# Kernel tuning notes

Hardware: AMD Instinct MI355X
Metric: run time of the kernel (lower is better)

Reference implementation:

```python
import jax, jax.numpy as jnp
import numpy as np

B, T, C, H, MAX_LEN = 16, 512, 1024, 16, 512
D = C // H  # head_dim = 64

def setup_inputs() -> dict:
    key = jax.random.key(0)
    ks = jax.random.split(key, 10)
    s = 1.0 / np.sqrt(C)
    return {
        "x": jax.random.normal(ks[0], (B, T, C), dtype=jnp.float32),
        "Wq": jax.random.normal(ks[1], (C, C), dtype=jnp.float32) * s,
        "bq": jnp.zeros((C,), dtype=jnp.float32),
        "Wk": jax.random.normal(ks[2], (C, C), dtype=jnp.float32) * s,
        "bk": jnp.zeros((C,), dtype=jnp.float32),
        "Wv": jax.random.normal(ks[3], (C, C), dtype=jnp.float32) * s,
        "bv": jnp.zeros((C,), dtype=jnp.float32),
        "Wo": jax.random.normal(ks[4], (C, C), dtype=jnp.float32) * s,
        "bo": jnp.zeros((C,), dtype=jnp.float32),
        "rel_pos_bias": jax.random.normal(ks[5], (H, MAX_LEN, MAX_LEN), dtype=jnp.float32) * 0.02,
    }

def reference(x, Wq, bq, Wk, bk, Wv, bv, Wo, bo, rel_pos_bias):
    scale = 1.0 / jnp.sqrt(jnp.float32(D))
    # projections (torch Linear: x @ W.T + b), reshape to (B,H,T,D)
    def proj(W, b):
        return (x @ W.T + b).reshape(B, T, H, D).transpose(0, 2, 1, 3)
    q, k, v = proj(Wq, bq), proj(Wk, bk), proj(Wv, bv)
    attn = jnp.einsum('bhtd,bhsd->bhts', q, k) * scale  # (B,H,T,T)
    attn = attn + rel_pos_bias[None, :, :T, :T]
    causal = jnp.triu(jnp.ones((T, T), dtype=bool), k=1)
    attn = jnp.where(causal[None, None], -jnp.inf, attn)
    attn = jax.nn.softmax(attn, axis=-1)  # dropout p=0 (eval) -> identity
    out = jnp.einsum('bhts,bhsd->bhtd', attn, v)
    out = out.transpose(0, 2, 1, 3).reshape(B, T, C)
    return out @ Wo.T + bo
```

## Files before the change

### kernel.cpp

```cpp
#include <hip/hip_runtime.h>
#include <stdint.h>
#include <math.h>

#define DEV static __device__ __forceinline__

typedef __attribute__((ext_vector_type(8))) __bf16 bf16x8;
typedef __attribute__((ext_vector_type(4))) float f32x4;
typedef unsigned short u16;

DEV u16 f2b(float f) {
  union { float f; uint32_t u; } x; x.f = f;
  uint32_t r = x.u + 0x7fffu + ((x.u >> 16) & 1u);
  return (u16)(r >> 16);
}

DEV uint32_t pk2(float a, float b) {
  return (uint32_t)f2b(a) | ((uint32_t)f2b(b) << 16);
}

DEV float b2f_lo(uint32_t u) { return __uint_as_float(u << 16); }
DEV float b2f_hi(uint32_t u) { return __uint_as_float(u & 0xffff0000u); }

DEV void glds16(const void* g, void* l) {
  __builtin_amdgcn_global_load_lds(
      (const __attribute__((address_space(1))) void*)g,
      (__attribute__((address_space(3))) void*)l, 16, 0, 0);
}

DEV f32x4 mfma16(bf16x8 a, bf16x8 b, f32x4 c) {
  return __builtin_amdgcn_mfma_f32_16x16x32_bf16(a, b, c, 0, 0, 0);
}

__global__ __launch_bounds__(256) void cvt_all(
    const float* __restrict__ x, const float* __restrict__ Wq,
    const float* __restrict__ Wk, const float* __restrict__ Wv,
    const float* __restrict__ Wo, const float* __restrict__ bias,
    u16* __restrict__ xb, u16* __restrict__ wqkv, u16* __restrict__ wo,
    u16* __restrict__ biasb) {
  size_t i = ((size_t)blockIdx.x * 256 + threadIdx.x) * 4;
  const float* s;
  u16* d;
  size_t off;
  float scale = 1.0f;
  if (i < 8388608)        { s = x;  d = xb;             off = i; }
  else if (i < 9437184)   { s = Wq; d = wqkv;           off = i - 8388608; }
  else if (i < 10485760)  { s = Wk; d = wqkv + 1048576; off = i - 9437184; }
  else if (i < 11534336)  { s = Wv; d = wqkv + 2097152; off = i - 10485760; }
  else if (i < 12582912)  { s = Wo; d = wo;             off = i - 11534336; }
  else { s = bias; d = biasb; off = i - 12582912; scale = 1.44269504f; }
  float4 v = *(const float4*)(s + off);
  ushort4 o;
  o.x = f2b(v.x * scale); o.y = f2b(v.y * scale);
  o.z = f2b(v.z * scale); o.w = f2b(v.w * scale);
  *(ushort4*)(d + off) = o;
}

__global__ __launch_bounds__(256) void gemm_qkv(
    const u16* __restrict__ A, const u16* __restrict__ Bw,
    const float* __restrict__ bq, const float* __restrict__ bk,
    const float* __restrict__ bv,
    u16* __restrict__ qo, u16* __restrict__ ko, u16* __restrict__ vto) {
  __shared__ u16 lsA[2][128 * 32];
  __shared__ u16 lsB[2][128 * 32];
  const int K = 1024;
  int tid = threadIdx.x, wave = tid >> 6, lane = tid & 63;
  int q16 = lane >> 4, c16 = lane & 15;
  int m0 = blockIdx.y * 128, n0 = blockIdx.x * 128;
  int wm = wave >> 1, wn = wave & 1;
  const bool vblk = (n0 >= 2048);
  const u16* lsR = vblk ? &lsB[0][0] : &lsA[0][0];
  const u16* lsC = vblk ? &lsA[0][0] : &lsB[0][0];
  int wr = vblk ? wn : wm;
  int wc = vblk ? wm : wn;

  f32x4 acc[4][4];
#pragma unroll
  for (int i = 0; i < 4; ++i)
#pragma unroll
    for (int j = 0; j < 4; ++j) acc[i][j] = (f32x4)0.0f;

  int srow = (lane >> 2);
  int scol = ((lane & 3) ^ ((lane >> 3) & 3)) * 8;
  int swz = (q16 ^ ((c16 >> 1) & 3)) * 8;

  for (int k0 = 0; k0 < K; k0 += 64) {
    __syncthreads();
#pragma unroll
    for (int half = 0; half < 2; ++half) {
#pragma unroll
      for (int cc = 0; cc < 2; ++cc) {
        int chunk = wave * 2 + cc;
        int r = chunk * 16 + srow;
        glds16(A + (size_t)(m0 + r) * K + k0 + half * 32 + scol,
               &lsA[half][chunk * 512]);
        glds16(Bw + (size_t)(n0 + r) * K + k0 + half * 32 + scol,
               &lsB[half][chunk * 512]);
      }
    }
    __syncthreads();
#pragma unroll
    for (int half = 0; half < 2; ++half) {
      bf16x8 rf[4], cf[4];
#pragma unroll
      for (int i = 0; i < 4; ++i)
        rf[i] = *(const bf16x8*)&lsR[half * 4096 +
                                     (wr * 64 + i * 16 + c16) * 32 + swz];
#pragma unroll
      for (int i = 0; i < 4; ++i)
        cf[i] = *(const bf16x8*)&lsC[half * 4096 +
                                     (wc * 64 + i * 16 + c16) * 32 + swz];
#pragma unroll
      for (int it = 0; it < 4; ++it)
#pragma unroll
        for (int jt = 0; jt < 4; ++jt)
          acc[it][jt] = mfma16(rf[it], cf[jt], acc[it][jt]);
    }
  }

  if (!vblk) {
#pragma unroll
    for (int mt = 0; mt < 4; ++mt) {
#pragma unroll
      for (int nt = 0; nt < 4; ++nt) {
        int n = n0 + wn * 64 + nt * 16 + c16;
        int which = n >> 10;
        int nl = n & 1023;
        int hh = nl >> 6, d = nl & 63;
        float bias = (which == 0 ? bq : bk)[nl];
        u16* dst = (which == 0 ? qo : ko);
#pragma unroll
        for (int r = 0; r < 4; ++r) {
          int m = m0 + wm * 64 + mt * 16 + q16 * 4 + r;
          int b = m >> 9, t = m & 511;
          size_t bh = (size_t)b * 16 + hh;
          dst[(bh * 512 + t) * 72 + d] = f2b(acc[mt][nt][r] + bias);
        }
      }
    }
  } else {
#pragma unroll
    for (int it = 0; it < 4; ++it) {
      int nbase = n0 + wn * 64 + it * 16 + q16 * 4;
      float4 bvv = *(const float4*)(bv + (nbase & 1023));
#pragma unroll
      for (int jt = 0; jt < 4; ++jt) {
        int m = m0 + wm * 64 + jt * 16 + c16;
        int b = m >> 9, t = m & 511;
        size_t bh4 = ((size_t)b * 16) * 4;
#pragma unroll
        for (int r = 0; r < 4; ++r) {
          int nl = (nbase + r) & 1023;
          int hh = nl >> 6, d = nl & 63;
          float bias = ((const float*)&bvv)[r];
          vto[((bh4 + (size_t)hh * 4 + (t >> 7)) * 64 + d) * 136 + (t & 127)] =
              f2b(acc[it][jt][r] + bias);
        }
      }
    }
  }
}

__global__ __launch_bounds__(256, 3) void attn_kernel(
    const u16* __restrict__ qglob, const u16* __restrict__ kglob,
    const u16* __restrict__ vtglob, const u16* __restrict__ biasb,
    u16* __restrict__ og) {
  __shared__ u16 lsK[128 * 72];
  __shared__ u16 lsV[64 * 136];
  __shared__ u16 lsP[4 * 32 * 72];

  int tid = threadIdx.x, wave = tid >> 6, lane = tid & 63;
  int q16 = lane >> 4, c16 = lane & 15;
  int bh = blockIdx.y;
  int b = bh >> 4, h = bh & 15;
  int bx = blockIdx.x;
  int q0 = bx * 128;

  const u16* qbase = qglob + (size_t)bh * (512 * 72) + (size_t)q0 * 72;
  const u16* kbase = kglob + (size_t)bh * (512 * 72);
  const u16* vbase = vtglob + (size_t)bh * 4 * (64 * 136);
  u16* lsPw = lsP + wave * (32 * 72);

  for (int i = wave; i < 18; i += 4)
    glds16(qbase + (size_t)i * 512 + lane * 8, lsK + i * 512);
  __syncthreads();
  bf16x8 qf[2][2];
#pragma unroll
  for (int nt = 0; nt < 2; ++nt)
#pragma unroll
    for (int ks = 0; ks < 2; ++ks)
      qf[nt][ks] = *(const bf16x8*)&lsK[(wave * 32 + nt * 16 + c16) * 72 +
                                        ks * 32 + q16 * 8];

  f32x4 oacc[2][4];
#pragma unroll
  for (int i = 0; i < 2; ++i)
#pragma unroll
    for (int j = 0; j < 4; ++j) oacc[i][j] = (f32x4)0.0f;
  float mold[2] = {-INFINITY, -INFINITY};
  float lsum[2] = {0.0f, 0.0f};
  const float SCL = 0.18033688f;

  for (int st = 0; st <= bx; ++st) {
    bool diag = (st == bx);
    __syncthreads();
    const u16* kt = kbase + (size_t)st * (128 * 72);
    for (int i = wave; i < 18; i += 4)
      glds16(kt + (size_t)i * 512 + lane * 8, lsK + i * 512);
    const u16* vt = vbase + (size_t)st * (64 * 136);
    for (int i = wave; i < 17; i += 4)
      glds16(vt + (size_t)i * 512 + lane * 8, lsV + i * 512);

    uint2 ub[2][8];
#pragma unroll
    for (int nt = 0; nt < 2; ++nt) {
      int qgl = q0 + wave * 32 + nt * 16 + c16;
      const u16* bp = biasb + ((size_t)h * 512 + qgl) * 512 + st * 128 + q16 * 4;
#pragma unroll
      for (int mt = 0; mt < 8; ++mt) ub[nt][mt] = *(const uint2*)(bp + mt * 16);
    }
    __syncthreads();

    f32x4 sa[8][2];
#pragma unroll
    for (int mt = 0; mt < 8; ++mt) {
      sa[mt][0] = (f32x4)0.0f;
      sa[mt][1] = (f32x4)0.0f;
    }
    int mtmax = diag ? 2 * wave + 2 : 8;
#pragma unroll
    for (int mt = 0; mt < 8; ++mt) {
      if (mt < mtmax) {
#pragma unroll
        for (int ks = 0; ks < 2; ++ks) {
          bf16x8 kf =
              *(const bf16x8*)&lsK[(mt * 16 + c16) * 72 + ks * 32 + q16 * 8];
          sa[mt][0] = mfma16(kf, qf[0][ks], sa[mt][0]);
          sa[mt][1] = mfma16(kf, qf[1][ks], sa[mt][1]);
        }
      }
    }

    float alpha[2];
#pragma unroll
    for (int nt = 0; nt < 2; ++nt) {
#pragma unroll
      for (int mt = 0; mt < 8; ++mt) {
        uint32_t lo = ub[nt][mt].x, hi = ub[nt][mt].y;
        f32x4 bv;
        bv[0] = b2f_lo(lo); bv[1] = b2f_hi(lo);
        bv[2] = b2f_lo(hi); bv[3] = b2f_hi(hi);
        sa[mt][nt] = sa[mt][nt] * SCL + bv;
      }
      if (diag) {
#pragma unroll
        for (int mt = 0; mt < 8; ++mt) {
          int d0 = mt * 16 + q16 * 4 - wave * 32 - nt * 16 - c16;
#pragma unroll
          for (int r = 0; r < 4; ++r)
            if (d0 + r > 0) sa[mt][nt][r] = -INFINITY;
        }
      }
      f32x4 m4 = sa[0][nt];
#pragma unroll
      for (int mt = 1; mt < 8; ++mt) {
        f32x4 v = sa[mt][nt];
        m4[0] = fmaxf(m4[0], v[0]); m4[1] = fmaxf(m4[1], v[1]);
        m4[2] = fmaxf(m4[2], v[2]); m4[3] = fmaxf(m4[3], v[3]);
      }
      float mx = fmaxf(fmaxf(m4[0], m4[1]), fmaxf(m4[2], m4[3]));
      mx = fmaxf(mx, __shfl_xor(mx, 16));
      mx = fmaxf(mx, __shfl_xor(mx, 32));
      float mnew = fmaxf(mold[nt], mx);
      alpha[nt] = exp2f(mold[nt] - mnew);
      mold[nt] = mnew;
      f32x4 s4 = (f32x4)0.0f;
#pragma unroll
      for (int mt = 0; mt < 8; ++mt) {
        f32x4 p;
        p[0] = exp2f(sa[mt][nt][0] - mnew);
        p[1] = exp2f(sa[mt][nt][1] - mnew);
        p[2] = exp2f(sa[mt][nt][2] - mnew);
        p[3] = exp2f(sa[mt][nt][3] - mnew);
        sa[mt][nt] = p;
        s4 += p;
      }
      float ss = (s4[0] + s4[1]) + (s4[2] + s4[3]);
      ss += __shfl_xor(ss, 16);
      ss += __shfl_xor(ss, 32);
      lsum[nt] = lsum[nt] * alpha[nt] + ss;
    }

#pragma unroll
    for (int mo = 0; mo < 2; ++mo) {
      f32x4 av;
#pragma unroll
      for (int r = 0; r < 4; ++r) av[r] = __shfl(alpha[mo], q16 * 4 + r);
#pragma unroll
      for (int dt = 0; dt < 4; ++dt) oacc[mo][dt] *= av;
    }

    int G = diag ? wave + 1 : 4;
#pragma unroll
    for (int hf = 0; hf < 2; ++hf) {
      if (hf * 2 < G) {
#pragma unroll
        for (int nt = 0; nt < 2; ++nt)
#pragma unroll
          for (int mt4 = 0; mt4 < 4; ++mt4) {
            f32x4 p = sa[hf * 4 + mt4][nt];
            uint2 w;
            w.x = pk2(p[0], p[1]);
            w.y = pk2(p[2], p[3]);
            *(uint2*)&lsPw[(nt * 16 + c16) * 72 + mt4 * 16 + q16 * 4] = w;
          }
#pragma unroll
        for (int ksh = 0; ksh < 2; ++ksh) {
          if (hf * 2 + ksh < G) {
            bf16x8 pf0 =
                *(const bf16x8*)&lsPw[c16 * 72 + ksh * 32 + q16 * 8];
            bf16x8 pf1 =
                *(const bf16x8*)&lsPw[(16 + c16) * 72 + ksh * 32 + q16 * 8];
#pragma unroll
            for (int dt = 0; dt < 4; ++dt) {
              bf16x8 vf = *(const bf16x8*)&lsV[(dt * 16 + c16) * 136 +
                                               hf * 64 + ksh * 32 + q16 * 8];
              oacc[0][dt] = mfma16(pf0, vf, oacc[0][dt]);
              oacc[1][dt] = mfma16(pf1, vf, oacc[1][dt]);
            }
          }
        }
      }
    }
  }

#pragma unroll
  for (int mo = 0; mo < 2; ++mo) {
    f32x4 lv;
#pragma unroll
    for (int r = 0; r < 4; ++r) lv[r] = __shfl(lsum[mo], q16 * 4 + r);
#pragma unroll
    for (int r = 0; r < 4; ++r) {
      int tg = q0 + wave * 32 + mo * 16 + q16 * 4 + r;
      float inv = 1.0f / lv[r];
#pragma unroll
      for (int dt = 0; dt < 4; ++dt)
        og[((size_t)b * 512 + tg) * 1024 + h * 64 + dt * 16 + c16] =
            f2b(oacc[mo][dt][r] * inv);
    }
  }
}

__global__ __launch_bounds__(256) void gemm_out(
    const u16* __restrict__ A, const u16* __restrict__ W,
    const float* __restrict__ bo, float* __restrict__ out) {
  __shared__ u16 lsA[2][128 * 32];
  __shared__ u16 lsB[2][128 * 32];
  const int K = 1024;
  int tid = threadIdx.x, wave = tid >> 6, lane = tid & 63;
  int q16 = lane >> 4, c16 = lane & 15;
  int m0 = blockIdx.y * 128, n0 = blockIdx.x * 128;
  int wm = wave >> 1, wn = wave & 1;

  f32x4 acc[4][4];
#pragma unroll
  for (int i = 0; i < 4; ++i)
#pragma unroll
    for (int j = 0; j < 4; ++j) acc[i][j] = (f32x4)0.0f;

  int srow = (lane >> 2);
  int scol = ((lane & 3) ^ ((lane >> 3) & 3)) * 8;
  int swz = (q16 ^ ((c16 >> 1) & 3)) * 8;

  for (int k0 = 0; k0 < K; k0 += 64) {
    __syncthreads();
#pragma unroll
    for (int half = 0; half < 2; ++half) {
#pragma unroll
      for (int cc = 0; cc < 2; ++cc) {
        int chunk = wave * 2 + cc;
        int r = chunk * 16 + srow;
        glds16(A + (size_t)(m0 + r) * K + k0 + half * 32 + scol,
               &lsA[half][chunk * 512]);
        glds16(W + (size_t)(n0 + r) * K + k0 + half * 32 + scol,
               &lsB[half][chunk * 512]);
      }
    }
    __syncthreads();
#pragma unroll
    for (int half = 0; half < 2; ++half) {
      bf16x8 af[4], bf[4];
#pragma unroll
      for (int i = 0; i < 4; ++i)
        af[i] = *(const bf16x8*)&lsA[half][(wm * 64 + i * 16 + c16) * 32 + swz];
#pragma unroll
      for (int i = 0; i < 4; ++i)
        bf[i] = *(const bf16x8*)&lsB[half][(wn * 64 + i * 16 + c16) * 32 + swz];
#pragma unroll
      for (int mt = 0; mt < 4; ++mt)
#pragma unroll
        for (int nt = 0; nt < 4; ++nt)
          acc[mt][nt] = mfma16(af[mt], bf[nt], acc[mt][nt]);
    }
  }

#pragma unroll
  for (int mt = 0; mt < 4; ++mt) {
#pragma unroll
    for (int nt = 0; nt < 4; ++nt) {
      int n = n0 + wn * 64 + nt * 16 + c16;
      float bias = bo[n];
#pragma unroll
      for (int r = 0; r < 4; ++r) {
        int m = m0 + wm * 64 + mt * 16 + q16 * 4 + r;
        out[(size_t)m * 1024 + n] = acc[mt][nt][r] + bias;
      }
    }
  }
}

extern "C" void kernel_launch(void* const* d_in, const int* in_sizes, int n_in,
                              void* d_out, int out_size, void* d_ws, size_t ws_size,
                              hipStream_t stream) {
  const float* x    = (const float*)d_in[0];
  const float* Wq   = (const float*)d_in[1];
  const float* bq   = (const float*)d_in[2];
  const float* Wk   = (const float*)d_in[3];
  const float* bk   = (const float*)d_in[4];
  const float* Wv   = (const float*)d_in[5];
  const float* bv   = (const float*)d_in[6];
  const float* Wo   = (const float*)d_in[7];
  const float* bo   = (const float*)d_in[8];
  const float* bias = (const float*)d_in[9];
  float* out = (float*)d_out;

  const size_t MB = 1u << 20;
  char* ws = (char*)d_ws;
  u16* xb    = (u16*)(ws);
  u16* wqkv  = (u16*)(ws + 16 * MB);
  u16* wo    = (u16*)(ws + 22 * MB);
  u16* biasb = (u16*)(ws + 24 * MB);
  u16* qb    = (u16*)(ws + 32 * MB);
  u16* kb    = (u16*)(ws + 50 * MB);
  u16* vtb   = (u16*)(ws + 68 * MB);
  u16* ab    = xb;

  cvt_all<<<16384, 256, 0, stream>>>(x, Wq, Wk, Wv, Wo, bias,
                                     xb, wqkv, wo, biasb);
  gemm_qkv<<<dim3(24, 64), 256, 0, stream>>>(xb, wqkv, bq, bk, bv, qb, kb, vtb);
  attn_kernel<<<dim3(4, 256), 256, 0, stream>>>(qb, kb, vtb, biasb, ab);
  gemm_out<<<dim3(8, 64), 256, 0, stream>>>(ab, wo, bo, out);
}
```

Before: 289.7 us.

## Split attention block into eight waves of sixteen query rows each

Reworks the attention kernel to run 512 threads per block, with each wave owning 16 query rows instead of 32. Per-wave accumulator and score register arrays are halved and launch bounds are raised to target higher occupancy. The diagonal causal skipping becomes finer-grained. In exchange, each K and V fragment read from LDS now feeds a single MFMA, so the ratio of LDS reads to FLOPs doubles.

```diff
diff --git a/kernel.cpp b/kernel.cpp
--- a/kernel.cpp
+++ b/kernel.cpp
@@ -160,13 +160,13 @@
   }
 }
 
-__global__ __launch_bounds__(256, 3) void attn_kernel(
+__global__ __launch_bounds__(512, 6) void attn_kernel(
     const u16* __restrict__ qglob, const u16* __restrict__ kglob,
     const u16* __restrict__ vtglob, const u16* __restrict__ biasb,
     u16* __restrict__ og) {
   __shared__ u16 lsK[128 * 72];
   __shared__ u16 lsV[64 * 136];
-  __shared__ u16 lsP[4 * 32 * 72];
+  __shared__ u16 lsP[8 * 16 * 72];
 
   int tid = threadIdx.x, wave = tid >> 6, lane = tid & 63;
   int q16 = lane >> 4, c16 = lane & 15;
@@ -178,55 +178,46 @@
   const u16* qbase = qglob + (size_t)bh * (512 * 72) + (size_t)q0 * 72;
   const u16* kbase = kglob + (size_t)bh * (512 * 72);
   const u16* vbase = vtglob + (size_t)bh * 4 * (64 * 136);
-  u16* lsPw = lsP + wave * (32 * 72);
-
-  for (int i = wave; i < 18; i += 4)
+  u16* lsPw = lsP + wave * (16 * 72);
+
+  for (int i = wave; i < 18; i += 8)
     glds16(qbase + (size_t)i * 512 + lane * 8, lsK + i * 512);
   __syncthreads();
-  bf16x8 qf[2][2];
-#pragma unroll
-  for (int nt = 0; nt < 2; ++nt)
-#pragma unroll
-    for (int ks = 0; ks < 2; ++ks)
-      qf[nt][ks] = *(const bf16x8*)&lsK[(wave * 32 + nt * 16 + c16) * 72 +
-                                        ks * 32 + q16 * 8];
-
-  f32x4 oacc[2][4];
-#pragma unroll
-  for (int i = 0; i < 2; ++i)
-#pragma unroll
-    for (int j = 0; j < 4; ++j) oacc[i][j] = (f32x4)0.0f;
-  float mold[2] = {-INFINITY, -INFINITY};
-  float lsum[2] = {0.0f, 0.0f};
+  bf16x8 qf[2];
+#pragma unroll
+  for (int ks = 0; ks < 2; ++ks)
+    qf[ks] = *(const bf16x8*)&lsK[(wave * 16 + c16) * 72 + ks * 32 + q16 * 8];
+
+  f32x4 oacc[4];
+#pragma unroll
+  for (int j = 0; j < 4; ++j) oacc[j] = (f32x4)0.0f;
+  float mold = -INFINITY;
+  float lsum = 0.0f;
   const float SCL = 0.18033688f;
 
   for (int st = 0; st <= bx; ++st) {
     bool diag = (st == bx);
     __syncthreads();
     const u16* kt = kbase + (size_t)st * (128 * 72);
-    for (int i = wave; i < 18; i += 4)
+    for (int i = wave; i < 18; i += 8)
       glds16(kt + (size_t)i * 512 + lane * 8, lsK + i * 512);
     const u16* vt = vbase + (size_t)st * (64 * 136);
-    for (int i = wave; i < 17; i += 4)
+    for (int i = wave; i < 17; i += 8)
       glds16(vt + (size_t)i * 512 + lane * 8, lsV + i * 512);
 
-    uint2 ub[2][8];
-#pragma unroll
-    for (int nt = 0; nt < 2; ++nt) {
-      int qgl = q0 + wave * 32 + nt * 16 + c16;
+    uint2 ub[8];
+    {
+      int qgl = q0 + wave * 16 + c16;
       const u16* bp = biasb + ((size_t)h * 512 + qgl) * 512 + st * 128 + q16 * 4;
 #pragma unroll
-      for (int mt = 0; mt < 8; ++mt) ub[nt][mt] = *(const uint2*)(bp + mt * 16);
-    }
-    __syncthreads();
-
-    f32x4 sa[8][2];
-#pragma unroll
-    for (int mt = 0; mt < 8; ++mt) {
-      sa[mt][0] = (f32x4)0.0f;
-      sa[mt][1] = (f32x4)0.0f;
-    }
-    int mtmax = diag ? 2 * wave + 2 : 8;
+      for (int mt = 0; mt < 8; ++mt) ub[mt] = *(const uint2*)(bp + mt * 16);
+    }
+    __syncthreads();
+
+    f32x4 sa[8];
+#pragma unroll
+    for (int mt = 0; mt < 8; ++mt) sa[mt] = (f32x4)0.0f;
+    int mtmax = diag ? wave + 1 : 8;
 #pragma unroll
     for (int mt = 0; mt < 8; ++mt) {
       if (mt < mtmax) {
@@ -234,98 +225,87 @@
         for (int ks = 0; ks < 2; ++ks) {
           bf16x8 kf =
               *(const bf16x8*)&lsK[(mt * 16 + c16) * 72 + ks * 32 + q16 * 8];
-          sa[mt][0] = mfma16(kf, qf[0][ks], sa[mt][0]);
-          sa[mt][1] = mfma16(kf, qf[1][ks], sa[mt][1]);
+          sa[mt] = mfma16(kf, qf[ks], sa[mt]);
         }
       }
     }
 
-    float alpha[2];
-#pragma unroll
-    for (int nt = 0; nt < 2; ++nt) {
+#pragma unroll
+    for (int mt = 0; mt < 8; ++mt) {
+      uint32_t lo = ub[mt].x, hi = ub[mt].y;
+      f32x4 bv;
+      bv[0] = b2f_lo(lo); bv[1] = b2f_hi(lo);
+      bv[2] = b2f_lo(hi); bv[3] = b2f_hi(hi);
+      sa[mt] = sa[mt] * SCL + bv;
+    }
+    if (diag) {
 #pragma unroll
       for (int mt = 0; mt < 8; ++mt) {
-        uint32_t lo = ub[nt][mt].x, hi = ub[nt][mt].y;
-        f32x4 bv;
-        bv[0] = b2f_lo(lo); bv[1] = b2f_hi(lo);
-        bv[2] = b2f_lo(hi); bv[3] = b2f_hi(hi);
-        sa[mt][nt] = sa[mt][nt] * SCL + bv;
-      }
-      if (diag) {
-#pragma unroll
-        for (int mt = 0; mt < 8; ++mt) {
-          int d0 = mt * 16 + q16 * 4 - wave * 32 - nt * 16 - c16;
-#pragma unroll
-          for (int r = 0; r < 4; ++r)
-            if (d0 + r > 0) sa[mt][nt][r] = -INFINITY;
-        }
-      }
-      f32x4 m4 = sa[0][nt];
-#pragma unroll
-      for (int mt = 1; mt < 8; ++mt) {
-        f32x4 v = sa[mt][nt];
-        m4[0] = fmaxf(m4[0], v[0]); m4[1] = fmaxf(m4[1], v[1]);
-        m4[2] = fmaxf(m4[2], v[2]); m4[3] = fmaxf(m4[3], v[3]);
-      }
-      float mx = fmaxf(fmaxf(m4[0], m4[1]), fmaxf(m4[2], m4[3]));
-      mx = fmaxf(mx, __shfl_xor(mx, 16));
-      mx = fmaxf(mx, __shfl_xor(mx, 32));
-      float mnew = fmaxf(mold[nt], mx);
-      alpha[nt] = exp2f(mold[nt] - mnew);
-      mold[nt] = mnew;
-      f32x4 s4 = (f32x4)0.0f;
-#pragma unroll
-      for (int mt = 0; mt < 8; ++mt) {
-        f32x4 p;
-        p[0] = exp2f(sa[mt][nt][0] - mnew);
-        p[1] = exp2f(sa[mt][nt][1] - mnew);
-        p[2] = exp2f(sa[mt][nt][2] - mnew);
-        p[3] = exp2f(sa[mt][nt][3] - mnew);
-        sa[mt][nt] = p;
-        s4 += p;
-      }
-      float ss = (s4[0] + s4[1]) + (s4[2] + s4[3]);
-      ss += __shfl_xor(ss, 16);
-      ss += __shfl_xor(ss, 32);
-      lsum[nt] = lsum[nt] * alpha[nt] + ss;
-    }
-
-#pragma unroll
-    for (int mo = 0; mo < 2; ++mo) {
+        int d0 = mt * 16 + q16 * 4 - wave * 16 - c16;
+#pragma unroll
+        for (int r = 0; r < 4; ++r)
+          if (d0 + r > 0) sa[mt][r] = -INFINITY;
+      }
+    }
+
+    f32x4 m4 = sa[0];
+#pragma unroll
+    for (int mt = 1; mt < 8; ++mt) {
+      f32x4 v = sa[mt];
+      m4[0] = fmaxf(m4[0], v[0]); m4[1] = fmaxf(m4[1], v[1]);
+      m4[2] = fmaxf(m4[2], v[2]); m4[3] = fmaxf(m4[3], v[3]);
+    }
+    float mx = fmaxf(fmaxf(m4[0], m4[1]), fmaxf(m4[2], m4[3]));
+    mx = fmaxf(mx, __shfl_xor(mx, 16));
+    mx = fmaxf(mx, __shfl_xor(mx, 32));
+    float mnew = fmaxf(mold, mx);
+    float alpha = exp2f(mold - mnew);
+    mold = mnew;
+    f32x4 s4 = (f32x4)0.0f;
+#pragma unroll
+    for (int mt = 0; mt < 8; ++mt) {
+      f32x4 p;
+      p[0] = exp2f(sa[mt][0] - mnew);
+      p[1] = exp2f(sa[mt][1] - mnew);
+      p[2] = exp2f(sa[mt][2] - mnew);
+      p[3] = exp2f(sa[mt][3] - mnew);
+      sa[mt] = p;
+      s4 += p;
+    }
+    float ss = (s4[0] + s4[1]) + (s4[2] + s4[3]);
+    ss += __shfl_xor(ss, 16);
+    ss += __shfl_xor(ss, 32);
+    lsum = lsum * alpha + ss;
+
+    {
       f32x4 av;
 #pragma unroll
-      for (int r = 0; r < 4; ++r) av[r] = __shfl(alpha[mo], q16 * 4 + r);
-#pragma unroll
-      for (int dt = 0; dt < 4; ++dt) oacc[mo][dt] *= av;
-    }
-
-    int G = diag ? wave + 1 : 4;
+      for (int r = 0; r < 4; ++r) av[r] = __shfl(alpha, q16 * 4 + r);
+#pragma unroll
+      for (int dt = 0; dt < 4; ++dt) oacc[dt] *= av;
+    }
+
+    int G = diag ? (wave + 2) >> 1 : 4;
 #pragma unroll
     for (int hf = 0; hf < 2; ++hf) {
       if (hf * 2 < G) {
 #pragma unroll
-        for (int nt = 0; nt < 2; ++nt)
-#pragma unroll
-          for (int mt4 = 0; mt4 < 4; ++mt4) {
-            f32x4 p = sa[hf * 4 + mt4][nt];
-            uint2 w;
-            w.x = pk2(p[0], p[1]);
-            w.y = pk2(p[2], p[3]);
-            *(uint2*)&lsPw[(nt * 16 + c16) * 72 + mt4 * 16 + q16 * 4] = w;
-          }
+        for (int mt4 = 0; mt4 < 4; ++mt4) {
+          f32x4 p = sa[hf * 4 + mt4];
+          uint2 w;
+          w.x = pk2(p[0], p[1]);
+          w.y = pk2(p[2], p[3]);
+          *(uint2*)&lsPw[c16 * 72 + mt4 * 16 + q16 * 4] = w;
+        }
 #pragma unroll
         for (int ksh = 0; ksh < 2; ++ksh) {
           if (hf * 2 + ksh < G) {
-            bf16x8 pf0 =
-                *(const bf16x8*)&lsPw[c16 * 72 + ksh * 32 + q16 * 8];
-            bf16x8 pf1 =
-                *(const bf16x8*)&lsPw[(16 + c16) * 72 + ksh * 32 + q16 * 8];
+            bf16x8 pf = *(const bf16x8*)&lsPw[c16 * 72 + ksh * 32 + q16 * 8];
 #pragma unroll
             for (int dt = 0; dt < 4; ++dt) {
               bf16x8 vf = *(const bf16x8*)&lsV[(dt * 16 + c16) * 136 +
                                                hf * 64 + ksh * 32 + q16 * 8];
-              oacc[0][dt] = mfma16(pf0, vf, oacc[0][dt]);
-              oacc[1][dt] = mfma16(pf1, vf, oacc[1][dt]);
+              oacc[dt] = mfma16(pf, vf, oacc[dt]);
             }
           }
         }
@@ -333,20 +313,17 @@
     }
   }
 
-#pragma unroll
-  for (int mo = 0; mo < 2; ++mo) {
-    f32x4 lv;
-#pragma unroll
-    for (int r = 0; r < 4; ++r) lv[r] = __shfl(lsum[mo], q16 * 4 + r);
-#pragma unroll
-    for (int r = 0; r < 4; ++r) {
-      int tg = q0 + wave * 32 + mo * 16 + q16 * 4 + r;
-      float inv = 1.0f / lv[r];
-#pragma unroll
-      for (int dt = 0; dt < 4; ++dt)
-        og[((size_t)b * 512 + tg) * 1024 + h * 64 + dt * 16 + c16] =
-            f2b(oacc[mo][dt][r] * inv);
-    }
+  f32x4 lv;
+#pragma unroll
+  for (int r = 0; r < 4; ++r) lv[r] = __shfl(lsum, q16 * 4 + r);
+#pragma unroll
+  for (int r = 0; r < 4; ++r) {
+    int tg = q0 + wave * 16 + q16 * 4 + r;
+    float inv = 1.0f / lv[r];
+#pragma unroll
+    for (int dt = 0; dt < 4; ++dt)
+      og[((size_t)b * 512 + tg) * 1024 + h * 64 + dt * 16 + c16] =
+          f2b(oacc[dt][r] * inv);
   }
 }
 
@@ -447,6 +424,6 @@
   cvt_all<<<16384, 256, 0, stream>>>(x, Wq, Wk, Wv, Wo, bias,
                                      xb, wqkv, wo, biasb);
   gemm_qkv<<<dim3(24, 64), 256, 0, stream>>>(xb, wqkv, bq, bk, bv, qb, kb, vtb);
-  attn_kernel<<<dim3(4, 256), 256, 0, stream>>>(qb, kb, vtb, biasb, ab);
+  attn_kernel<<<dim3(4, 256), 512, 0, stream>>>(qb, kb, vtb, biasb, ab);
   gemm_out<<<dim3(8, 64), 256, 0, stream>>>(ab, wo, bo, out);
 }
```

Measured after the change: 361.6 us. +24.8%, slower.
